# Kernel tuning notes

Measured on AMD Instinct MI355X. Metric: run time of the kernel, lower is better.

## Reference

```python
import jax, jax.numpy as jnp
import numpy as np

W_POINT = 1.0
W_COEFF = 0.5
W_AFFINE = 0.5


def _euler_xyz_to_matrix(angles):
    # angles: [B, 3] Euler angles, XYZ convention: R = Rx @ Ry @ Rz (pytorch3d style)
    ax, ay, az = angles[:, 0], angles[:, 1], angles[:, 2]
    cx, sx = jnp.cos(ax), jnp.sin(ax)
    cy, sy = jnp.cos(ay), jnp.sin(ay)
    cz, sz = jnp.cos(az), jnp.sin(az)
    one = jnp.ones_like(cx)
    zero = jnp.zeros_like(cx)
    Rx = jnp.stack([one, zero, zero,
                    zero, cx, -sx,
                    zero, sx, cx], axis=-1).reshape(-1, 3, 3)
    Ry = jnp.stack([cy, zero, sy,
                    zero, one, zero,
                    -sy, zero, cy], axis=-1).reshape(-1, 3, 3)
    Rz = jnp.stack([cz, -sz, zero,
                    sz, cz, zero,
                    zero, zero, one], axis=-1).reshape(-1, 3, 3)
    return Rx @ Ry @ Rz


def _chamfer(pred, targ):
    # pred: [B,N,3], targ: [B,M,3]; symmetric chamfer of squared distances
    p2 = jnp.sum(pred * pred, axis=-1)        # [B,N]
    t2 = jnp.sum(targ * targ, axis=-1)        # [B,M]
    d2 = p2[:, :, None] + t2[:, None, :] - 2.0 * jnp.einsum('bnd,bmd->bnm', pred, targ)
    d2 = jnp.maximum(d2, 0.0)
    return jnp.mean(jnp.min(d2, axis=2)) + jnp.mean(jnp.min(d2, axis=1))


def setup_inputs() -> dict:
    key = jax.random.key(0)
    ks = jax.random.split(key, 6)
    B, N, M, K = 16, 4096, 4096, 128
    return {
        'pred_shape': jax.random.normal(ks[0], (B, N, 3), dtype=jnp.float32),
        'pred_weights': jax.random.normal(ks[1], (B, K), dtype=jnp.float32),
        'pred_affine': jax.random.uniform(ks[2], (B, 9), dtype=jnp.float32),
        'targ_shape': jax.random.normal(ks[3], (B, M, 3), dtype=jnp.float32),
        'targ_weights': jax.random.normal(ks[4], (B, K), dtype=jnp.float32),
        'targ_affine': jax.random.uniform(ks[5], (B, 9), dtype=jnp.float32),
    }


def reference(pred_shape, pred_weights, pred_affine, targ_shape, targ_weights, targ_affine):
    rot, trans, scale = targ_affine[:, 0:3], targ_affine[:, 3:6], targ_affine[:, 6:9]
    R = _euler_xyz_to_matrix(rot)                                   # [B,3,3]
    # row-vector convention (pytorch3d Transform3d): p' = (p @ R) * s + t
    targ_moving = jnp.einsum('bmd,bde->bme', targ_shape, R) * scale[:, None, :] + trans[:, None, :]
    point_loss = _chamfer(pred_shape, targ_moving)
    coeff_loss = jnp.mean((pred_weights - targ_weights) ** 2)
    affine_loss = jnp.mean((pred_affine - targ_affine) ** 2)
    total = W_POINT * point_loss + W_COEFF * coeff_loss + W_AFFINE * affine_loss
    return total, point_loss, coeff_loss, affine_loss
```

## Files before the change

kernel.cpp:

```cpp
#include <hip/hip_runtime.h>
#include <math.h>

#define BB 16
#define NN 4096
#define KK 128
#define NTILE 16
#define TS (NN / NTILE)
#define NCHUNK 2
#define QPT 8
#define TPB 256
#define W_POINT  1.0f
#define W_COEFF  0.5f
#define W_AFFINE 0.5f

__device__ inline void compute_affine(const float* __restrict__ aff,
                                      float R[9], float sc[3], float tr[3]) {
    float ax = aff[0], ay = aff[1], az = aff[2];
    tr[0] = aff[3]; tr[1] = aff[4]; tr[2] = aff[5];
    sc[0] = aff[6]; sc[1] = aff[7]; sc[2] = aff[8];
    float cx = cosf(ax), sx = sinf(ax);
    float cy = cosf(ay), sy = sinf(ay);
    float cz = cosf(az), sz = sinf(az);
    R[0] = cy * cz;                 R[1] = -cy * sz;                R[2] = sy;
    R[3] = cx * sz + sx * sy * cz;  R[4] = cx * cz - sx * sy * sz;  R[5] = -sx * cy;
    R[6] = sx * sz - cx * sy * cz;  R[7] = sx * cz + cx * sy * sz;  R[8] = cx * cy;
}

__device__ inline void apply_affine(const float R[9], const float sc[3], const float tr[3],
                                    float x, float y, float z,
                                    float& ox, float& oy, float& oz) {
    ox = fmaf(fmaf(x, R[0], fmaf(y, R[3], z * R[6])), sc[0], tr[0]);
    oy = fmaf(fmaf(x, R[1], fmaf(y, R[4], z * R[7])), sc[1], tr[1]);
    oz = fmaf(fmaf(x, R[2], fmaf(y, R[5], z * R[8])), sc[2], tr[2]);
}

__global__ __launch_bounds__(TPB, 4) void chamfer_kernel(
        const float* __restrict__ pred_shape,
        const float* __restrict__ targ_shape,
        const float* __restrict__ targ_affine,
        unsigned int* __restrict__ pmin) {
    __shared__ float4 lds[TS];

    const int bx    = blockIdx.x;
    const int tile  = bx & (NTILE - 1);
    const int chunk = (bx >> 4) & (NCHUNK - 1);
    const int b     = bx >> 5;
    const int dir   = blockIdx.y;
    const int tid   = threadIdx.x;

    float R[9], sc[3], tr[3];
    compute_affine(targ_affine + b * 9, R, sc, tr);

    {
        const int rbase = tile * TS;
        if (dir == 0) {
            const float* ts = targ_shape + ((size_t)b * NN + rbase + tid) * 3;
            float x = ts[0], y = ts[1], z = ts[2];
            float mx, my, mz;
            apply_affine(R, sc, tr, x, y, z, mx, my, mz);
            lds[tid] = make_float4(mx, my, mz, fmaf(mx, mx, fmaf(my, my, mz * mz)));
        } else {
            const float* ps = pred_shape + ((size_t)b * NN + rbase + tid) * 3;
            float x = ps[0], y = ps[1], z = ps[2];
            lds[tid] = make_float4(x, y, z, fmaf(x, x, fmaf(y, y, z * z)));
        }
    }
    __syncthreads();

    const int qbase = chunk * (TPB * QPT);
    float ax[QPT], ay[QPT], az[QPT], q2[QPT], mn[QPT];
    #pragma unroll
    for (int k = 0; k < QPT; ++k) {
        const int qi = qbase + k * TPB + tid;
        float x, y, z;
        if (dir == 0) {
            const float* p = pred_shape + ((size_t)b * NN + qi) * 3;
            x = p[0]; y = p[1]; z = p[2];
        } else {
            const float* t = targ_shape + ((size_t)b * NN + qi) * 3;
            apply_affine(R, sc, tr, t[0], t[1], t[2], x, y, z);
        }
        q2[k] = fmaf(x, x, fmaf(y, y, z * z));
        ax[k] = -2.0f * x; ay[k] = -2.0f * y; az[k] = -2.0f * z;
        mn[k] = 1e30f;
    }

    for (int j = 0; j < TS; j += 4) {
        float4 t0 = lds[j + 0], t1 = lds[j + 1], t2 = lds[j + 2], t3 = lds[j + 3];
        #pragma unroll
        for (int k = 0; k < QPT; ++k) {
            float v0 = fmaf(ax[k], t0.x, fmaf(ay[k], t0.y, fmaf(az[k], t0.z, t0.w)));
            float v1 = fmaf(ax[k], t1.x, fmaf(ay[k], t1.y, fmaf(az[k], t1.z, t1.w)));
            float v2 = fmaf(ax[k], t2.x, fmaf(ay[k], t2.y, fmaf(az[k], t2.z, t2.w)));
            float v3 = fmaf(ax[k], t3.x, fmaf(ay[k], t3.y, fmaf(az[k], t3.z, t3.w)));
            mn[k] = fminf(mn[k], fminf(fminf(v0, v1), fminf(v2, v3)));
        }
    }

    #pragma unroll
    for (int k = 0; k < QPT; ++k) {
        const int qi = qbase + k * TPB + tid;
        float d = fmaxf(q2[k] + mn[k], 0.0f);
        atomicMin(&pmin[((size_t)dir * BB + b) * NN + qi], __float_as_uint(d));
    }
}

__global__ __launch_bounds__(TPB) void reduce_pmin(
        const unsigned int* __restrict__ pmin,
        float* __restrict__ partials) {
    const int tid = threadIdx.x;
    const uint4* pm4 = (const uint4*)(pmin + (size_t)blockIdx.x * 4096);
    float ps = 0.0f;
    #pragma unroll
    for (int r = 0; r < 4; ++r) {
        uint4 u = pm4[r * TPB + tid];
        ps += __uint_as_float(u.x) + __uint_as_float(u.y)
            + __uint_as_float(u.z) + __uint_as_float(u.w);
    }
    #pragma unroll
    for (int off = 32; off > 0; off >>= 1) ps += __shfl_down(ps, off);
    __shared__ float sps[4];
    const int wid = tid >> 6;
    if ((tid & 63) == 0) sps[wid] = ps;
    __syncthreads();
    if (tid == 0) partials[blockIdx.x] = sps[0] + sps[1] + sps[2] + sps[3];
}

__global__ __launch_bounds__(TPB) void final_combine(
        const float* __restrict__ partials,
        const float* __restrict__ pred_w,  const float* __restrict__ targ_w,
        const float* __restrict__ pred_aff, const float* __restrict__ targ_aff,
        float* __restrict__ out) {
    const int tid = threadIdx.x;
    float ps = (tid < 32) ? partials[tid] : 0.0f;
    float cs = 0.0f;
    #pragma unroll
    for (int r = 0; r < (BB * KK) / TPB; ++r) {
        float d = pred_w[r * TPB + tid] - targ_w[r * TPB + tid];
        cs = fmaf(d, d, cs);
    }
    float as = 0.0f;
    if (tid < BB * 9) {
        float d = pred_aff[tid] - targ_aff[tid];
        as = d * d;
    }
    #pragma unroll
    for (int off = 32; off > 0; off >>= 1) {
        ps += __shfl_down(ps, off);
        cs += __shfl_down(cs, off);
        as += __shfl_down(as, off);
    }
    __shared__ float sps[4], scs[4], sas[4];
    const int wid = tid >> 6;
    if ((tid & 63) == 0) { sps[wid] = ps; scs[wid] = cs; sas[wid] = as; }
    __syncthreads();
    if (tid == 0) {
        float p = sps[0] + sps[1] + sps[2] + sps[3];
        float c = scs[0] + scs[1] + scs[2] + scs[3];
        float a = sas[0] + sas[1] + sas[2] + sas[3];
        float point  = p / (float)(BB * NN);
        float coeff  = c / (float)(BB * KK);
        float affine = a / (float)(BB * 9);
        out[0] = W_POINT * point + W_COEFF * coeff + W_AFFINE * affine;
        out[1] = point;
        out[2] = coeff;
        out[3] = affine;
    }
}

extern "C" void kernel_launch(void* const* d_in, const int* in_sizes, int n_in,
                              void* d_out, int out_size, void* d_ws, size_t ws_size,
                              hipStream_t stream) {
    const float* pred_shape = (const float*)d_in[0];
    const float* pred_w     = (const float*)d_in[1];
    const float* pred_aff   = (const float*)d_in[2];
    const float* targ_shape = (const float*)d_in[3];
    const float* targ_w     = (const float*)d_in[4];
    const float* targ_aff   = (const float*)d_in[5];
    float* out = (float*)d_out;
    unsigned int* pmin = (unsigned int*)d_ws;
    float* partials = (float*)(pmin + 2 * BB * NN);

    hipMemsetAsync(pmin, 0x7f, (size_t)2 * BB * NN * sizeof(unsigned int), stream);

    chamfer_kernel<<<dim3(BB * NCHUNK * NTILE, 2), TPB, 0, stream>>>(
        pred_shape, targ_shape, targ_aff, pmin);
    reduce_pmin<<<32, TPB, 0, stream>>>(pmin, partials);
    final_combine<<<1, TPB, 0, stream>>>(partials, pred_w, targ_w,
                                         pred_aff, targ_aff, out);
}
```

Measured before the change: 112.8 us.

## Compute both chamfer directions from one distance tile with rotating column mins

The kernel no longer runs the pred->targ and targ->pred passes separately. Each block computes a single 2048x128 distance tile and takes row minima in registers. Column minima are carried by a value that rotates across lanes via ds_bpermute, so each distance is evaluated once instead of twice. It also uses v_min3 inline assembly to cut min instructions. The cost is extra cross-lane permutes, per-wave column atomics, and more min work per iteration.

Result: faster. 101.9 us (-9.7%).

```diff
diff --git a/kernel.cpp b/kernel.cpp
--- a/kernel.cpp
+++ b/kernel.cpp
@@ -4,14 +4,21 @@
 #define BB 16
 #define NN 4096
 #define KK 128
-#define NTILE 16
-#define TS (NN / NTILE)
-#define NCHUNK 2
-#define QPT 8
+#define RT 2048
+#define CT 128
+#define RPT 8
 #define TPB 256
+#define NRTILE (NN / RT)
+#define NCTILE (NN / CT)
 #define W_POINT  1.0f
 #define W_COEFF  0.5f
 #define W_AFFINE 0.5f
+
+__device__ inline float min3f(float a, float b, float c) {
+    float r;
+    asm("v_min3_f32 %0, %1, %2, %3" : "=v"(r) : "v"(a), "v"(b), "v"(c));
+    return r;
+}
 
 __device__ inline void compute_affine(const float* __restrict__ aff,
                                       float R[9], float sc[3], float tr[3]) {
@@ -39,69 +46,78 @@
         const float* __restrict__ targ_shape,
         const float* __restrict__ targ_affine,
         unsigned int* __restrict__ pmin) {
-    __shared__ float4 lds[TS];
+    __shared__ float4 ldsc[CT];
 
     const int bx    = blockIdx.x;
-    const int tile  = bx & (NTILE - 1);
-    const int chunk = (bx >> 4) & (NCHUNK - 1);
-    const int b     = bx >> 5;
-    const int dir   = blockIdx.y;
+    const int ctile = bx & (NCTILE - 1);
+    const int rtile = (bx >> 5) & (NRTILE - 1);
+    const int b     = bx >> 6;
     const int tid   = threadIdx.x;
+    const int lane  = tid & 63;
 
     float R[9], sc[3], tr[3];
     compute_affine(targ_affine + b * 9, R, sc, tr);
 
-    {
-        const int rbase = tile * TS;
-        if (dir == 0) {
-            const float* ts = targ_shape + ((size_t)b * NN + rbase + tid) * 3;
-            float x = ts[0], y = ts[1], z = ts[2];
-            float mx, my, mz;
-            apply_affine(R, sc, tr, x, y, z, mx, my, mz);
-            lds[tid] = make_float4(mx, my, mz, fmaf(mx, mx, fmaf(my, my, mz * mz)));
-        } else {
-            const float* ps = pred_shape + ((size_t)b * NN + rbase + tid) * 3;
-            float x = ps[0], y = ps[1], z = ps[2];
-            lds[tid] = make_float4(x, y, z, fmaf(x, x, fmaf(y, y, z * z)));
-        }
-    }
-    __syncthreads();
-
-    const int qbase = chunk * (TPB * QPT);
-    float ax[QPT], ay[QPT], az[QPT], q2[QPT], mn[QPT];
-    #pragma unroll
-    for (int k = 0; k < QPT; ++k) {
-        const int qi = qbase + k * TPB + tid;
-        float x, y, z;
-        if (dir == 0) {
-            const float* p = pred_shape + ((size_t)b * NN + qi) * 3;
-            x = p[0]; y = p[1]; z = p[2];
-        } else {
-            const float* t = targ_shape + ((size_t)b * NN + qi) * 3;
-            apply_affine(R, sc, tr, t[0], t[1], t[2], x, y, z);
-        }
+    if (tid < CT) {
+        const float* t = targ_shape + ((size_t)b * NN + ctile * CT + tid) * 3;
+        float mx, my, mz;
+        apply_affine(R, sc, tr, t[0], t[1], t[2], mx, my, mz);
+        ldsc[tid] = make_float4(mx, my, mz, fmaf(mx, mx, fmaf(my, my, mz * mz)));
+    }
+
+    const int rowbase = rtile * RT;
+    float ax[RPT], ay[RPT], az[RPT], q2[RPT], rmin[RPT];
+    #pragma unroll
+    for (int k = 0; k < RPT; ++k) {
+        const float* p = pred_shape + ((size_t)b * NN + rowbase + k * TPB + tid) * 3;
+        float x = p[0], y = p[1], z = p[2];
         q2[k] = fmaf(x, x, fmaf(y, y, z * z));
         ax[k] = -2.0f * x; ay[k] = -2.0f * y; az[k] = -2.0f * z;
-        mn[k] = 1e30f;
-    }
-
-    for (int j = 0; j < TS; j += 4) {
-        float4 t0 = lds[j + 0], t1 = lds[j + 1], t2 = lds[j + 2], t3 = lds[j + 3];
+        rmin[k] = 1e30f;
+    }
+    __syncthreads();
+
+    float cr0 = 1e30f, cr1 = 1e30f;
+    const int rot = ((lane + 1) & 63) << 2;
+    for (int i = 0; i < 64; ++i) {
+        const int idx = (lane + i) & 63;
+        float4 t0 = ldsc[idx];
+        float4 t1 = ldsc[idx + 64];
+        float da[RPT], db[RPT];
         #pragma unroll
-        for (int k = 0; k < QPT; ++k) {
-            float v0 = fmaf(ax[k], t0.x, fmaf(ay[k], t0.y, fmaf(az[k], t0.z, t0.w)));
-            float v1 = fmaf(ax[k], t1.x, fmaf(ay[k], t1.y, fmaf(az[k], t1.z, t1.w)));
-            float v2 = fmaf(ax[k], t2.x, fmaf(ay[k], t2.y, fmaf(az[k], t2.z, t2.w)));
-            float v3 = fmaf(ax[k], t3.x, fmaf(ay[k], t3.y, fmaf(az[k], t3.z, t3.w)));
-            mn[k] = fminf(mn[k], fminf(fminf(v0, v1), fminf(v2, v3)));
+        for (int k = 0; k < RPT; ++k) {
+            float s0 = q2[k] + t0.w;
+            float s1 = q2[k] + t1.w;
+            float e0 = fmaf(ax[k], t0.x, fmaf(ay[k], t0.y, fmaf(az[k], t0.z, s0)));
+            float e1 = fmaf(ax[k], t1.x, fmaf(ay[k], t1.y, fmaf(az[k], t1.z, s1)));
+            rmin[k] = min3f(rmin[k], e0, e1);
+            da[k] = e0; db[k] = e1;
         }
-    }
-
-    #pragma unroll
-    for (int k = 0; k < QPT; ++k) {
-        const int qi = qbase + k * TPB + tid;
-        float d = fmaxf(q2[k] + mn[k], 0.0f);
-        atomicMin(&pmin[((size_t)dir * BB + b) * NN + qi], __float_as_uint(d));
+        float a0 = min3f(da[0], da[1], da[2]);
+        float b0 = min3f(da[3], da[4], da[5]);
+        float c0 = min3f(da[6], da[7], cr0);
+        cr0 = min3f(a0, b0, c0);
+        float a1 = min3f(db[0], db[1], db[2]);
+        float b1 = min3f(db[3], db[4], db[5]);
+        float c1 = min3f(db[6], db[7], cr1);
+        cr1 = min3f(a1, b1, c1);
+        cr0 = __int_as_float(__builtin_amdgcn_ds_bpermute(rot, __float_as_int(cr0)));
+        cr1 = __int_as_float(__builtin_amdgcn_ds_bpermute(rot, __float_as_int(cr1)));
+    }
+
+    #pragma unroll
+    for (int k = 0; k < RPT; ++k) {
+        float d = fmaxf(rmin[k], 0.0f);
+        atomicMin(&pmin[(size_t)b * NN + rowbase + k * TPB + tid],
+                  __float_as_uint(d));
+    }
+    {
+        float d0 = fmaxf(cr0, 0.0f);
+        atomicMin(&pmin[(size_t)(BB + b) * NN + ctile * CT + lane],
+                  __float_as_uint(d0));
+        float d1 = fmaxf(cr1, 0.0f);
+        atomicMin(&pmin[(size_t)(BB + b) * NN + ctile * CT + 64 + lane],
+                  __float_as_uint(d1));
     }
 }
 
@@ -183,7 +199,7 @@
 
     hipMemsetAsync(pmin, 0x7f, (size_t)2 * BB * NN * sizeof(unsigned int), stream);
 
-    chamfer_kernel<<<dim3(BB * NCHUNK * NTILE, 2), TPB, 0, stream>>>(
+    chamfer_kernel<<<dim3(BB * NRTILE * NCTILE), TPB, 0, stream>>>(
         pred_shape, targ_shape, targ_aff, pmin);
     reduce_pmin<<<32, TPB, 0, stream>>>(pmin, partials);
     final_combine<<<1, TPB, 0, stream>>>(partials, pred_w, targ_w,
```
